# Optimization experiments

Measured on AMD Instinct MI355X. Metric: run time of the kernel, lower is better.

The kernel has to match this reference:

```python
import jax, jax.numpy as jnp
import numpy as np

B, T, C, H, W = 2, 2048, 2048, 16, 512
D = C // H  # head_dim = 128

def setup_inputs() -> dict:
    key = jax.random.key(0)
    k1, k2, k3 = jax.random.split(key, 3)
    x = jax.random.normal(k1, (B, T, C), dtype=jnp.float32)
    w_attn = jax.random.normal(k2, (C, 3 * C), dtype=jnp.float32) * 0.02
    w_proj = jax.random.normal(k3, (C, C), dtype=jnp.float32) * 0.02
    # standard RoPE tables: [T, D] with halves repeated
    inv_freq = 1.0 / (10000.0 ** (jnp.arange(0, D, 2, dtype=jnp.float32) / D))
    freqs = jnp.outer(jnp.arange(T, dtype=jnp.float32), inv_freq)  # [T, D/2]
    emb = jnp.concatenate([freqs, freqs], axis=-1)  # [T, D]
    return {"x": x, "freqs_cos": jnp.cos(emb), "freqs_sin": jnp.sin(emb),
            "w_attn": w_attn, "w_proj": w_proj}

def _rotate_half(t):
    return jnp.concatenate([-t[..., D // 2:], t[..., :D // 2]], axis=-1)

def reference(x, freqs_cos, freqs_sin, w_attn, w_proj):
    qkv = x @ w_attn  # [B,T,3C]
    q, k, v = jnp.split(qkv, 3, axis=-1)
    # [B,T,C] -> [B,H,T,D]
    q = q.reshape(B, T, H, D).transpose(0, 2, 1, 3)
    k = k.reshape(B, T, H, D).transpose(0, 2, 1, 3)
    v = v.reshape(B, T, H, D).transpose(0, 2, 1, 3)
    cos = freqs_cos[None, None, :, :]  # [1,1,T,D]
    sin = freqs_sin[None, None, :, :]
    q = q * cos + _rotate_half(q) * sin
    k = k * cos + _rotate_half(k) * sin
    scores = jnp.einsum('bhqd,bhkd->bhqk', q, k) / jnp.sqrt(jnp.float32(D))
    i = jnp.arange(T)[:, None]
    j = jnp.arange(T)[None, :]
    band = (j <= i) & (j > i - W)  # causal sliding window of width W
    scores = jnp.where(band[None, None, :, :], scores, -jnp.inf)
    att = jax.nn.softmax(scores, axis=-1)
    y = jnp.einsum('bhqk,bhkd->bhqd', att, v)
    y = y.transpose(0, 2, 1, 3).reshape(B, T, C)
    return y @ w_proj
```

## Files before the change

kernel.cpp:

```cpp
#include <hip/hip_runtime.h>
#include <stdint.h>

#define B_ 2
#define T_ 2048
#define C_ 2048
#define H_ 16
#define D_ 128
#define W_ 512
#define M_ (B_*T_)
#define N1_ (3*C_)

typedef short bf16x8 __attribute__((ext_vector_type(8)));
typedef unsigned short u16x8 __attribute__((ext_vector_type(8)));
typedef float f32x4 __attribute__((ext_vector_type(4)));

#define SB() __builtin_amdgcn_sched_barrier(0)

__device__ __forceinline__ unsigned short f2bf(float f) {
  union { float f; unsigned u; } v; v.f = f;
  unsigned r = v.u + 0x7fffu + ((v.u >> 16) & 1u);
  return (unsigned short)(r >> 16);
}
__device__ __forceinline__ float bf2f(unsigned short b) {
  union { unsigned u; float f; } v; v.u = ((unsigned)b) << 16;
  return v.f;
}

__device__ __forceinline__ void gload_lds16(const void* g, void* l) {
  __builtin_amdgcn_global_load_lds((const __attribute__((address_space(1))) void*)g,
                                   (__attribute__((address_space(3))) void*)l, 16, 0, 0);
}

__global__ void k_cvt(const float* __restrict__ s, unsigned short* __restrict__ d, int n) {
  int i = (blockIdx.x * blockDim.x + threadIdx.x) * 8;
  if (i >= n) return;
  float4 a = *(const float4*)(s + i);
  float4 b = *(const float4*)(s + i + 4);
  u16x8 o;
  o[0]=f2bf(a.x); o[1]=f2bf(a.y); o[2]=f2bf(a.z); o[3]=f2bf(a.w);
  o[4]=f2bf(b.x); o[5]=f2bf(b.y); o[6]=f2bf(b.z); o[7]=f2bf(b.w);
  *(u16x8*)(d + i) = o;
}

__global__ void k_tcvt(const float* __restrict__ s, unsigned short* __restrict__ d, int R, int Cc) {
  __shared__ float tile[32][33];
  int c0 = blockIdx.x * 32, r0 = blockIdx.y * 32;
  int tx = threadIdx.x & 31, ty = threadIdx.x >> 5;
  #pragma unroll
  for (int j = 0; j < 32; j += 8) tile[ty + j][tx] = s[(size_t)(r0 + ty + j) * Cc + c0 + tx];
  __syncthreads();
  #pragma unroll
  for (int j = 0; j < 32; j += 8) d[(size_t)(c0 + ty + j) * R + r0 + tx] = f2bf(tile[tx][ty + j]);
}

template<int ROWS, int K>
__device__ __forceinline__ void stage_half(const unsigned short* __restrict__ gbase,
                                           int row0, int kt, int kh,
                                           unsigned short* region, int tid, int sw) {
  const char* gsrc = (const char*)(gbase + (size_t)row0 * K + kt * 64 + kh * 32);
  {
    int o = tid * 16, s = o ^ sw;
    gload_lds16(gsrc + (size_t)(s >> 6) * (K * 2) + (s & 63), (char*)region + o);
  }
  if (ROWS == 256) {
    int o = (512 + tid) * 16, s = o ^ sw;
    gload_lds16(gsrc + (size_t)(s >> 6) * (K * 2) + (s & 63), (char*)region + o);
  }
}

template<bool F32OUT, int K, int Ntot>
__global__ __launch_bounds__(512, 2) void k_gemm8(const unsigned short* __restrict__ A,
                                                  const unsigned short* __restrict__ Bt,
                                                  void* __restrict__ Cp) {
  __shared__ unsigned short As[2][2][256 * 32];
  __shared__ unsigned short Bs[2][2][256 * 32];
  const int tid = threadIdx.x, lane = tid & 63, wv = tid >> 6;
  const int wm = wv >> 2, wn = wv & 3;
  const int lr = lane & 15, lg = lane >> 4;
  const int sw = tid & 32;
  const int fofs = lr * 64 + ((lg * 16) ^ ((lr & 8) << 2));
  const int aoff = wm * 128 * 64 + fofs;
  const int boff = wn * 64 * 64 + fofs;

  const int nwg = gridDim.x;
  const int nbx = Ntot >> 8;
  const int q = nwg >> 3, r = nwg & 7;
  const int xcd = blockIdx.x & 7, off = blockIdx.x >> 3;
  const int bid = (xcd < r ? xcd * (q + 1) : r * (q + 1) + (xcd - r) * q) + off;
  const int bm0 = (bid / nbx) << 8;
  const int bn0 = (bid % nbx) << 8;

  f32x4 acc[8][4];
  #pragma unroll
  for (int i = 0; i < 8; ++i)
    #pragma unroll
    for (int j = 0; j < 4; ++j)
      #pragma unroll
      for (int e = 0; e < 4; ++e) acc[i][j][e] = 0.f;

  constexpr int NT = K >> 6;

  stage_half<256, K>(A,  bm0, 0, 0, As[0][0], tid, sw);
  stage_half<256, K>(Bt, bn0, 0, 0, Bs[0][0], tid, sw);
  stage_half<256, K>(Bt, bn0, 0, 1, Bs[0][1], tid, sw);
  stage_half<256, K>(A,  bm0, 0, 1, As[0][1], tid, sw);
  stage_half<256, K>(Bt, bn0, 1, 0, Bs[1][0], tid, sw);
  stage_half<256, K>(A,  bm0, 1, 0, As[1][0], tid, sw);
  stage_half<256, K>(Bt, bn0, 1, 1, Bs[1][1], tid, sw);
  asm volatile("s_waitcnt vmcnt(4)" ::: "memory");
  __builtin_amdgcn_s_barrier();

  bf16x8 Xa[4], Xb[4], Ya[4];
  #pragma unroll
  for (int j = 0; j < 4; ++j) Xb[j] = *(const bf16x8*)((const char*)Bs[0][0] + boff + j * 1024);
  #pragma unroll
  for (int i = 0; i < 4; ++i) Xa[i] = *(const bf16x8*)((const char*)As[0][0] + aoff + i * 1024);

  #pragma unroll 2
  for (int t = 0; t < NT; ++t) {
    const int p = t & 1;
    asm volatile("s_waitcnt lgkmcnt(0)" ::: "memory");
    SB();
    __builtin_amdgcn_s_setprio(1);
    #pragma unroll
    for (int i = 0; i < 4; ++i)
      #pragma unroll
      for (int j = 0; j < 4; ++j)
        acc[i][j] = __builtin_amdgcn_mfma_f32_16x16x32_bf16(Xa[i], Xb[j], acc[i][j], 0, 0, 0);
    __builtin_amdgcn_s_setprio(0);
    #pragma unroll
    for (int i = 0; i < 4; ++i) Ya[i] = *(const bf16x8*)((const char*)As[p][0] + aoff + (i + 4) * 1024);
    if (t + 1 < NT) stage_half<256, K>(A, bm0, t + 1, 1, As[p ^ 1][1], tid, sw);
    __builtin_amdgcn_s_barrier();

    asm volatile("s_waitcnt lgkmcnt(0)" ::: "memory");
    SB();
    __builtin_amdgcn_s_setprio(1);
    #pragma unroll
    for (int i = 0; i < 4; ++i)
      #pragma unroll
      for (int j = 0; j < 4; ++j)
        acc[i + 4][j] = __builtin_amdgcn_mfma_f32_16x16x32_bf16(Ya[i], Xb[j], acc[i + 4][j], 0, 0, 0);
    __builtin_amdgcn_s_setprio(0);
    #pragma unroll
    for (int j = 0; j < 4; ++j) Xb[j] = *(const bf16x8*)((const char*)Bs[p][1] + boff + j * 1024);
    #pragma unroll
    for (int i = 0; i < 4; ++i) Xa[i] = *(const bf16x8*)((const char*)As[p][1] + aoff + i * 1024);
    if (t + 2 < NT) stage_half<256, K>(Bt, bn0, t + 2, 0, Bs[p][0], tid, sw);
    __builtin_amdgcn_s_barrier();

    asm volatile("s_waitcnt lgkmcnt(0)" ::: "memory");
    SB();
    __builtin_amdgcn_s_setprio(1);
    #pragma unroll
    for (int i = 0; i < 4; ++i)
      #pragma unroll
      for (int j = 0; j < 4; ++j)
        acc[i][j] = __builtin_amdgcn_mfma_f32_16x16x32_bf16(Xa[i], Xb[j], acc[i][j], 0, 0, 0);
    __builtin_amdgcn_s_setprio(0);
    #pragma unroll
    for (int i = 0; i < 4; ++i) Ya[i] = *(const bf16x8*)((const char*)As[p][1] + aoff + (i + 4) * 1024);
    if (t + 2 < NT) stage_half<256, K>(A, bm0, t + 2, 0, As[p][0], tid, sw);
    __builtin_amdgcn_s_barrier();

    asm volatile("s_waitcnt lgkmcnt(0)" ::: "memory");
    SB();
    __builtin_amdgcn_s_setprio(1);
    #pragma unroll
    for (int i = 0; i < 4; ++i)
      #pragma unroll
      for (int j = 0; j < 4; ++j)
        acc[i + 4][j] = __builtin_amdgcn_mfma_f32_16x16x32_bf16(Ya[i], Xb[j], acc[i + 4][j], 0, 0, 0);
    __builtin_amdgcn_s_setprio(0);
    if (t < NT - 2) asm volatile("s_waitcnt vmcnt(4)" ::: "memory");
    else            asm volatile("s_waitcnt vmcnt(0)" ::: "memory");
    #pragma unroll
    for (int j = 0; j < 4; ++j) Xb[j] = *(const bf16x8*)((const char*)Bs[p ^ 1][0] + boff + j * 1024);
    #pragma unroll
    for (int i = 0; i < 4; ++i) Xa[i] = *(const bf16x8*)((const char*)As[p ^ 1][0] + aoff + i * 1024);
    if (t + 2 < NT) stage_half<256, K>(Bt, bn0, t + 2, 1, Bs[p][1], tid, sw);
    __builtin_amdgcn_s_barrier();
  }
  asm volatile("s_waitcnt lgkmcnt(0)" ::: "memory");

  #pragma unroll
  for (int i = 0; i < 8; ++i)
    #pragma unroll
    for (int j = 0; j < 4; ++j) {
      int m = bm0 + wm * 128 + i * 16 + lg * 4;
      int n = bn0 + wn * 64 + j * 16 + lr;
      #pragma unroll
      for (int e = 0; e < 4; ++e) {
        if (F32OUT) ((float*)Cp)[(size_t)(m + e) * Ntot + n] = acc[i][j][e];
        else ((unsigned short*)Cp)[(size_t)(m + e) * Ntot + n] = f2bf(acc[i][j][e]);
      }
    }
}

template<bool F32OUT, int K, int Ntot>
__global__ __launch_bounds__(512, 1) void k_gemmT(const unsigned short* __restrict__ A,
                                                  const unsigned short* __restrict__ Bt,
                                                  void* __restrict__ Cp) {
  __shared__ unsigned short As[3][2][128 * 32];
  __shared__ unsigned short Bs[3][2][256 * 32];
  const int tid = threadIdx.x, lane = tid & 63, wv = tid >> 6;
  const int wm = wv >> 2, wn = wv & 3;
  const int lr = lane & 15, lg = lane >> 4;
  const int sw = tid & 32;
  const int fofs = lr * 64 + ((lg * 16) ^ ((lr & 8) << 2));
  const int aoff = wm * 64 * 64 + fofs;
  const int boff = wn * 64 * 64 + fofs;

  const int nwg = gridDim.x;
  const int nbx = Ntot >> 8;
  const int q = nwg >> 3, r = nwg & 7;
  const int xcd = blockIdx.x & 7, off = blockIdx.x >> 3;
  const int bid = (xcd < r ? xcd * (q + 1) : r * (q + 1) + (xcd - r) * q) + off;
  const int bm0 = (bid / nbx) * 128;
  const int bn0 = (bid % nbx) << 8;

  f32x4 acc[4][4];
  #pragma unroll
  for (int i = 0; i < 4; ++i)
    #pragma unroll
    for (int j = 0; j < 4; ++j)
      #pragma unroll
      for (int e = 0; e < 4; ++e) acc[i][j][e] = 0.f;

  constexpr int NT = K >> 6;

  auto stage_tile = [&](int kt, int rr) {
    stage_half<128, K>(A,  bm0, kt, 0, As[rr][0], tid, sw);
    stage_half<256, K>(Bt, bn0, kt, 0, Bs[rr][0], tid, sw);
    stage_half<128, K>(A,  bm0, kt, 1, As[rr][1], tid, sw);
    stage_half<256, K>(Bt, bn0, kt, 1, Bs[rr][1], tid, sw);
  };

  stage_tile(0, 0);
  stage_tile(1, 1);
  asm volatile("s_waitcnt vmcnt(6)" ::: "memory");
  __builtin_amdgcn_s_barrier();
  bf16x8 Pf[4], Qf[4], Xf[4], Yf[4];
  #pragma unroll
  for (int i = 0; i < 4; ++i) Pf[i] = *(const bf16x8*)((const char*)As[0][0] + aoff + i * 1024);
  #pragma unroll
  for (int j = 0; j < 4; ++j) Xf[j] = *(const bf16x8*)((const char*)Bs[0][0] + boff + j * 1024);

  int cur = 0;
  for (int t = 0; t < NT; ++t) {
    int rn = cur + 1; if (rn == 3) rn = 0;
    int rs = rn + 1; if (rs == 3) rs = 0;

    asm volatile("s_waitcnt lgkmcnt(0)" ::: "memory");
    SB();
    __builtin_amdgcn_s_setprio(1);
    #pragma unroll
    for (int i = 0; i < 4; ++i)
      #pragma unroll
      for (int j = 0; j < 4; ++j)
        acc[i][j] = __builtin_amdgcn_mfma_f32_16x16x32_bf16(Pf[i], Xf[j], acc[i][j], 0, 0, 0);
    __builtin_amdgcn_s_setprio(0);
    #pragma unroll
    for (int i = 0; i < 4; ++i) Qf[i] = *(const bf16x8*)((const char*)As[cur][1] + aoff + i * 1024);
    #pragma unroll
    for (int j = 0; j < 4; ++j) Yf[j] = *(const bf16x8*)((const char*)Bs[cur][1] + boff + j * 1024);
    if (t + 2 < NT) {
      stage_tile(t + 2, rs);
      asm volatile("s_waitcnt vmcnt(9)" ::: "memory");
    } else if (t + 1 < NT) {
      asm volatile("s_waitcnt vmcnt(3)" ::: "memory");
    } else {
      asm volatile("s_waitcnt vmcnt(0)" ::: "memory");
    }
    __builtin_amdgcn_s_barrier();

    asm volatile("s_waitcnt lgkmcnt(0)" ::: "memory");
    SB();
    __builtin_amdgcn_s_setprio(1);
    #pragma unroll
    for (int i = 0; i < 4; ++i)
      #pragma unroll
      for (int j = 0; j < 4; ++j)
        acc[i][j] = __builtin_amdgcn_mfma_f32_16x16x32_bf16(Qf[i], Yf[j], acc[i][j], 0, 0, 0);
    __builtin_amdgcn_s_setprio(0);
    if (t + 1 < NT) {
      #pragma unroll
      for (int i = 0; i < 4; ++i) Pf[i] = *(const bf16x8*)((const char*)As[rn][0] + aoff + i * 1024);
      #pragma unroll
      for (int j = 0; j < 4; ++j) Xf[j] = *(const bf16x8*)((const char*)Bs[rn][0] + boff + j * 1024);
    }
    if (t + 2 < NT) asm volatile("s_waitcnt vmcnt(6)" ::: "memory");
    else            asm volatile("s_waitcnt vmcnt(0)" ::: "memory");
    __builtin_amdgcn_s_barrier();

    cur = rn;
  }
  asm volatile("s_waitcnt lgkmcnt(0)" ::: "memory");

  #pragma unroll
  for (int i = 0; i < 4; ++i)
    #pragma unroll
    for (int j = 0; j < 4; ++j) {
      int m = bm0 + wm * 64 + i * 16 + lg * 4;
      int n = bn0 + wn * 64 + j * 16 + lr;
      #pragma unroll
      for (int e = 0; e < 4; ++e) {
        if (F32OUT) ((float*)Cp)[(size_t)(m + e) * Ntot + n] = acc[i][j][e];
        else ((unsigned short*)Cp)[(size_t)(m + e) * Ntot + n] = f2bf(acc[i][j][e]);
      }
    }
}

__global__ __launch_bounds__(256) void k_reorg(const unsigned short* __restrict__ qkv,
                        const float* __restrict__ fcos, const float* __restrict__ fsin,
                        unsigned short* __restrict__ q_r, unsigned short* __restrict__ k_r,
                        unsigned short* __restrict__ v_t) {
  const int bh = blockIdx.x, b = bh >> 4, h = bh & 15;
  const int t0 = blockIdx.y * 64;
  const int tid = threadIdx.x;
  __shared__ unsigned short vt[64][136];
  #pragma unroll
  for (int p = 0; p < 4; ++p) {
    int idx = p * 256 + tid;
    int tl = idx >> 4, sg = idx & 15;
    int t = t0 + tl, d0 = sg * 8;
    float sgn = (d0 < 64) ? -1.f : 1.f;
    float4 c0v = *(const float4*)(fcos + t * D_ + d0);
    float4 c1v = *(const float4*)(fcos + t * D_ + d0 + 4);
    float4 s0v = *(const float4*)(fsin + t * D_ + d0);
    float4 s1v = *(const float4*)(fsin + t * D_ + d0 + 4);
    float cs[8] = {c0v.x,c0v.y,c0v.z,c0v.w,c1v.x,c1v.y,c1v.z,c1v.w};
    float sn[8] = {s0v.x,s0v.y,s0v.z,s0v.w,s1v.x,s1v.y,s1v.z,s1v.w};
    #pragma unroll
    for (int w = 0; w < 2; ++w) {
      const unsigned short* src = qkv + (size_t)(b*T_ + t) * N1_ + w*C_ + h*D_;
      u16x8 a  = *(const u16x8*)(src + d0);
      u16x8 pr = *(const u16x8*)(src + (d0 ^ 64));
      u16x8 o;
      #pragma unroll
      for (int e = 0; e < 8; ++e)
        o[e] = f2bf(bf2f(a[e]) * cs[e] + sgn * bf2f(pr[e]) * sn[e]);
      unsigned short* dst = (w ? k_r : q_r) + (size_t)((b*H_ + h)*T_ + t) * D_ + d0;
      *(u16x8*)dst = o;
    }
    const unsigned short* vsrc = qkv + (size_t)(b*T_ + t) * N1_ + 2*C_ + h*D_ + d0;
    *(u16x8*)&vt[tl][d0] = *(const u16x8*)vsrc;
  }
  __syncthreads();
  #pragma unroll
  for (int p = 0; p < 4; ++p) {
    int idx = p * 256 + tid;
    int sg = idx & 7, d = idx >> 3;
    u16x8 o;
    #pragma unroll
    for (int e = 0; e < 8; ++e) o[e] = vt[sg*8 + e][d];
    *(u16x8*)(v_t + (size_t)((b*H_ + h)*D_ + d) * T_ + t0 + sg*8) = o;
  }
}

__global__ __launch_bounds__(512) void k_attn(const unsigned short* __restrict__ q_r,
                       const unsigned short* __restrict__ k_r,
                       const unsigned short* __restrict__ v_t,
                       unsigned short* __restrict__ y) {
  const int bh = blockIdx.x, b = bh >> 4, h = bh & 15;
  const int q0 = blockIdx.y * 128;
  const int tid = threadIdx.x, lane = tid & 63, wv = tid >> 6;
  const int lr = lane & 15, lg = lane >> 4;

  __shared__ unsigned short Ks[2][64 * 128];
  __shared__ unsigned short Vs[128 * 64];
  __shared__ unsigned short Ps[8 * 16 * 64];

  const size_t bhT = (size_t)(b*H_ + h) * T_;
  const size_t bhD = (size_t)(b*H_ + h) * D_;
  const unsigned short* qbase = q_r + (bhT + q0 + wv*16 + lr) * D_;
  bf16x8 qf[4];
  #pragma unroll
  for (int kk = 0; kk < 4; ++kk) qf[kk] = *(const bf16x8*)(qbase + kk*32 + lg*8);

  f32x4 o[8];
  #pragma unroll
  for (int i = 0; i < 8; ++i)
    #pragma unroll
    for (int e = 0; e < 4; ++e) o[i][e] = 0.f;
  float m_run[4], l_sum[4];
  #pragma unroll
  for (int e = 0; e < 4; ++e) { m_run[e] = -1e30f; l_sum[e] = 0.f; }

  const int i_min = q0 + wv*16, i_max = i_min + 15;
  int kt_lo = q0 - (W_ - 1); if (kt_lo < 0) kt_lo = 0; kt_lo &= ~63;
  const float scale = 0.08838834764831845f;

  unsigned short* Ps_w = Ps + wv * 1024;

  auto stage_k = [&](int kt, int buf) {
    #pragma unroll
    for (int c = 0; c < 2; ++c) {
      int ob = (c * 512 + tid) * 16;
      int row = ob >> 8, slot = (ob >> 4) & 15;
      int cb = slot ^ ((row & 7) << 1);
      gload_lds16(k_r + (bhT + kt + row) * D_ + cb * 8, (char*)Ks[buf] + ob);
    }
  };
  auto stage_v = [&](int kt) {
    #pragma unroll
    for (int c = 0; c < 2; ++c) {
      int ob = (c * 512 + tid) * 16;
      int d = ob >> 7, slot = (ob >> 4) & 7;
      int cb = slot ^ (d & 7);
      gload_lds16(v_t + (bhD + d) * T_ + kt + cb * 8, (char*)Vs + ob);
    }
  };

  stage_k(kt_lo, 0);
  int cur = 0;
  for (int kt = kt_lo; kt < q0 + 128; kt += 64) {
    const bool has_next = (kt + 64 < q0 + 128);
    stage_v(kt);
    if (has_next) stage_k(kt + 64, cur ^ 1);
    if (has_next) asm volatile("s_waitcnt vmcnt(4)" ::: "memory");
    else          asm volatile("s_waitcnt vmcnt(2)" ::: "memory");
    __builtin_amdgcn_s_barrier();

    const bool live = (kt <= i_max) && (kt + 63 >= i_min - (W_ - 1));
    float sv[4][4];
    if (live) {
      const unsigned short* Kc = Ks[cur];
      f32x4 s[4];
      #pragma unroll
      for (int ct = 0; ct < 4; ++ct)
        #pragma unroll
        for (int e = 0; e < 4; ++e) s[ct][e] = 0.f;
      #pragma unroll
      for (int kk = 0; kk < 4; ++kk) {
        #pragma unroll
        for (int ct = 0; ct < 4; ++ct) {
          bf16x8 kf = *(const bf16x8*)&Kc[(ct*16 + lr)*128 + ((kk*4 + lg) ^ ((lr & 7) << 1))*8];
          s[ct] = __builtin_amdgcn_mfma_f32_16x16x32_bf16(qf[kk], kf, s[ct], 0, 0, 0);
        }
      }
      float mnew[4];
      int grow = 0;
      #pragma unroll
      for (int e = 0; e < 4; ++e) {
        int i = i_min + lg*4 + e;
        float rm = -1e30f;
        #pragma unroll
        for (int ct = 0; ct < 4; ++ct) {
          int j = kt + ct*16 + lr;
          bool ok = (j <= i) && (j > i - W_);
          sv[e][ct] = ok ? s[ct][e] * scale : -1e30f;
          rm = fmaxf(rm, sv[e][ct]);
        }
        #pragma unroll
        for (int msk = 1; msk < 16; msk <<= 1) rm = fmaxf(rm, __shfl_xor(rm, msk));
        mnew[e] = fmaxf(m_run[e], rm);
        grow |= (mnew[e] > m_run[e]) ? 1 : 0;
      }
      if (__any(grow)) {
        #pragma unroll
        for (int e = 0; e < 4; ++e) {
          float fac = __expf(m_run[e] - mnew[e]);
          l_sum[e] *= fac;
          m_run[e] = mnew[e];
          #pragma unroll
          for (int nt = 0; nt < 8; ++nt) o[nt][e] *= fac;
        }
      }
      #pragma unroll
      for (int e = 0; e < 4; ++e) {
        int prow = lg*4 + e;
        float rs = 0.f;
        #pragma unroll
        for (int ct = 0; ct < 4; ++ct) {
          float pv = (sv[e][ct] > -1e29f) ? __expf(sv[e][ct] - m_run[e]) : 0.f;
          rs += pv;
          Ps_w[prow*64 + ((ct*2 + (lr >> 3)) ^ (prow & 7))*8 + (lr & 7)] = f2bf(pv);
        }
        #pragma unroll
        for (int msk = 1; msk < 16; msk <<= 1) rs += __shfl_xor(rs, msk);
        l_sum[e] += rs;
      }
    }
    if (has_next) asm volatile("s_waitcnt vmcnt(2)" ::: "memory");
    else          asm volatile("s_waitcnt vmcnt(0)" ::: "memory");
    __builtin_amdgcn_s_barrier();

    if (live) {
      asm volatile("s_waitcnt lgkmcnt(0)" ::: "memory"); SB();
      #pragma unroll
      for (int kk = 0; kk < 2; ++kk) {
        bf16x8 pf = *(const bf16x8*)&Ps_w[lr*64 + ((kk*4 + lg) ^ (lr & 7))*8];
        #pragma unroll
        for (int nt = 0; nt < 8; ++nt) {
          bf16x8 vf = *(const bf16x8*)&Vs[(nt*16 + lr)*64 + ((kk*4 + lg) ^ (lr & 7))*8];
          o[nt] = __builtin_amdgcn_mfma_f32_16x16x32_bf16(pf, vf, o[nt], 0, 0, 0);
        }
      }
    }
    asm volatile("s_waitcnt lgkmcnt(0)" ::: "memory");
    __builtin_amdgcn_s_barrier();
    cur ^= 1;
  }

  #pragma unroll
  for (int nt = 0; nt < 8; ++nt) {
    #pragma unroll
    for (int e = 0; e < 4; ++e) {
      int t = q0 + wv*16 + lg*4 + e;
      int d = nt*16 + lr;
      y[(size_t)(b*T_ + t) * C_ + h*D_ + d] = f2bf(o[nt][e] / l_sum[e]);
    }
  }
}

extern "C" void kernel_launch(void* const* d_in, const int* in_sizes, int n_in,
                              void* d_out, int out_size, void* d_ws, size_t ws_size,
                              hipStream_t stream) {
  const float* x      = (const float*)d_in[0];
  const float* fcos   = (const float*)d_in[1];
  const float* fsin   = (const float*)d_in[2];
  const float* w_attn = (const float*)d_in[3];
  const float* w_proj = (const float*)d_in[4];
  float* out = (float*)d_out;

  char* ws = (char*)d_ws;
  unsigned short* x_bf = (unsigned short*)(ws);
  unsigned short* wa_t = (unsigned short*)(ws + 16777216ull);
  unsigned short* wp_t = (unsigned short*)(ws + 41943040ull);
  unsigned short* qkv  = (unsigned short*)(ws + 50331648ull);
  unsigned short* q_r  = (unsigned short*)(ws + 100663296ull);
  unsigned short* k_r  = (unsigned short*)(ws + 117440512ull);
  unsigned short* v_t  = (unsigned short*)(ws + 134217728ull);
  unsigned short* y_bf = x_bf;

  k_cvt<<<dim3(4096), dim3(256), 0, stream>>>(x, x_bf, M_*C_);
  k_tcvt<<<dim3(192, 64), dim3(256), 0, stream>>>(w_attn, wa_t, C_, N1_);
  k_tcvt<<<dim3(64, 64), dim3(256), 0, stream>>>(w_proj, wp_t, C_, C_);
  k_gemm8<false, C_, N1_><<<dim3(384), dim3(512), 0, stream>>>(x_bf, wa_t, qkv);
  k_reorg<<<dim3(32, 32), dim3(256), 0, stream>>>(qkv, fcos, fsin, q_r, k_r, v_t);
  k_attn<<<dim3(32, 16), dim3(512), 0, stream>>>(q_r, k_r, v_t, y_bf);
  k_gemmT<true, C_, C_><<<dim3(256), dim3(512), 0, stream>>>(y_bf, wp_t, out);
}
```

Baseline: 283.3 us.

## Replace output projection GEMM with smaller 128x128 tile double-buffered kernel

The output projection GEMM moves from a 128x256 tile with a 3-stage software-pipelined register-prefetch loop to a 128x128 tile with a simple 2-stage LDS double buffer. The grid doubles to 512 workgroups and launch bounds allow several blocks per CU. The aim is to spread the 4096x2048 GEMM across more workgroups (256 only roughly matches the CU count) and gain occupancy-based latency hiding. The cost is losing the explicit register prefetch and vmcnt-overlapped scheduling, plus lower per-tile data reuse.

```diff
diff --git a/kernel.cpp b/kernel.cpp
--- a/kernel.cpp
+++ b/kernel.cpp
@@ -197,31 +197,31 @@
     }
 }
 
-template<bool F32OUT, int K, int Ntot>
-__global__ __launch_bounds__(512, 1) void k_gemmT(const unsigned short* __restrict__ A,
+template<int K, int Ntot>
+__global__ __launch_bounds__(512, 4) void k_gemmS(const unsigned short* __restrict__ A,
                                                   const unsigned short* __restrict__ Bt,
-                                                  void* __restrict__ Cp) {
-  __shared__ unsigned short As[3][2][128 * 32];
-  __shared__ unsigned short Bs[3][2][256 * 32];
+                                                  float* __restrict__ Cp) {
+  __shared__ unsigned short As[2][2][128 * 32];
+  __shared__ unsigned short Bs[2][2][128 * 32];
   const int tid = threadIdx.x, lane = tid & 63, wv = tid >> 6;
-  const int wm = wv >> 2, wn = wv & 3;
+  const int wm = wv >> 1, wn = wv & 1;
   const int lr = lane & 15, lg = lane >> 4;
   const int sw = tid & 32;
   const int fofs = lr * 64 + ((lg * 16) ^ ((lr & 8) << 2));
-  const int aoff = wm * 64 * 64 + fofs;
+  const int aoff = wm * 32 * 64 + fofs;
   const int boff = wn * 64 * 64 + fofs;
 
   const int nwg = gridDim.x;
-  const int nbx = Ntot >> 8;
+  const int nbx = Ntot >> 7;
   const int q = nwg >> 3, r = nwg & 7;
   const int xcd = blockIdx.x & 7, off = blockIdx.x >> 3;
   const int bid = (xcd < r ? xcd * (q + 1) : r * (q + 1) + (xcd - r) * q) + off;
-  const int bm0 = (bid / nbx) * 128;
-  const int bn0 = (bid % nbx) << 8;
-
-  f32x4 acc[4][4];
-  #pragma unroll
-  for (int i = 0; i < 4; ++i)
+  const int bm0 = (bid / nbx) << 7;
+  const int bn0 = (bid % nbx) << 7;
+
+  f32x4 acc[2][4];
+  #pragma unroll
+  for (int i = 0; i < 2; ++i)
     #pragma unroll
     for (int j = 0; j < 4; ++j)
       #pragma unroll
@@ -231,83 +231,49 @@
 
   auto stage_tile = [&](int kt, int rr) {
     stage_half<128, K>(A,  bm0, kt, 0, As[rr][0], tid, sw);
-    stage_half<256, K>(Bt, bn0, kt, 0, Bs[rr][0], tid, sw);
+    stage_half<128, K>(Bt, bn0, kt, 0, Bs[rr][0], tid, sw);
     stage_half<128, K>(A,  bm0, kt, 1, As[rr][1], tid, sw);
-    stage_half<256, K>(Bt, bn0, kt, 1, Bs[rr][1], tid, sw);
+    stage_half<128, K>(Bt, bn0, kt, 1, Bs[rr][1], tid, sw);
   };
 
   stage_tile(0, 0);
-  stage_tile(1, 1);
-  asm volatile("s_waitcnt vmcnt(6)" ::: "memory");
+  asm volatile("s_waitcnt vmcnt(0)" ::: "memory");
   __builtin_amdgcn_s_barrier();
-  bf16x8 Pf[4], Qf[4], Xf[4], Yf[4];
-  #pragma unroll
-  for (int i = 0; i < 4; ++i) Pf[i] = *(const bf16x8*)((const char*)As[0][0] + aoff + i * 1024);
-  #pragma unroll
-  for (int j = 0; j < 4; ++j) Xf[j] = *(const bf16x8*)((const char*)Bs[0][0] + boff + j * 1024);
-
-  int cur = 0;
+
   for (int t = 0; t < NT; ++t) {
-    int rn = cur + 1; if (rn == 3) rn = 0;
-    int rs = rn + 1; if (rs == 3) rs = 0;
-
-    asm volatile("s_waitcnt lgkmcnt(0)" ::: "memory");
-    SB();
-    __builtin_amdgcn_s_setprio(1);
-    #pragma unroll
-    for (int i = 0; i < 4; ++i)
-      #pragma unroll
-      for (int j = 0; j < 4; ++j)
-        acc[i][j] = __builtin_amdgcn_mfma_f32_16x16x32_bf16(Pf[i], Xf[j], acc[i][j], 0, 0, 0);
-    __builtin_amdgcn_s_setprio(0);
-    #pragma unroll
-    for (int i = 0; i < 4; ++i) Qf[i] = *(const bf16x8*)((const char*)As[cur][1] + aoff + i * 1024);
-    #pragma unroll
-    for (int j = 0; j < 4; ++j) Yf[j] = *(const bf16x8*)((const char*)Bs[cur][1] + boff + j * 1024);
-    if (t + 2 < NT) {
-      stage_tile(t + 2, rs);
-      asm volatile("s_waitcnt vmcnt(9)" ::: "memory");
-    } else if (t + 1 < NT) {
-      asm volatile("s_waitcnt vmcnt(3)" ::: "memory");
-    } else {
-      asm volatile("s_waitcnt vmcnt(0)" ::: "memory");
-    }
-    __builtin_amdgcn_s_barrier();
-
-    asm volatile("s_waitcnt lgkmcnt(0)" ::: "memory");
-    SB();
-    __builtin_amdgcn_s_setprio(1);
-    #pragma unroll
-    for (int i = 0; i < 4; ++i)
-      #pragma unroll
-      for (int j = 0; j < 4; ++j)
-        acc[i][j] = __builtin_amdgcn_mfma_f32_16x16x32_bf16(Qf[i], Yf[j], acc[i][j], 0, 0, 0);
-    __builtin_amdgcn_s_setprio(0);
-    if (t + 1 < NT) {
-      #pragma unroll
-      for (int i = 0; i < 4; ++i) Pf[i] = *(const bf16x8*)((const char*)As[rn][0] + aoff + i * 1024);
-      #pragma unroll
-      for (int j = 0; j < 4; ++j) Xf[j] = *(const bf16x8*)((const char*)Bs[rn][0] + boff + j * 1024);
-    }
-    if (t + 2 < NT) asm volatile("s_waitcnt vmcnt(6)" ::: "memory");
-    else            asm volatile("s_waitcnt vmcnt(0)" ::: "memory");
-    __builtin_amdgcn_s_barrier();
-
-    cur = rn;
-  }
-  asm volatile("s_waitcnt lgkmcnt(0)" ::: "memory");
-
-  #pragma unroll
-  for (int i = 0; i < 4; ++i)
+    const int p = t & 1;
+    if (t + 1 < NT) stage_tile(t + 1, p ^ 1);
+
+    bf16x8 af[2], bfr[4];
+    #pragma unroll
+    for (int kh = 0; kh < 2; ++kh) {
+      #pragma unroll
+      for (int i = 0; i < 2; ++i) af[i] = *(const bf16x8*)((const char*)As[p][kh] + aoff + i * 1024);
+      #pragma unroll
+      for (int j = 0; j < 4; ++j) bfr[j] = *(const bf16x8*)((const char*)Bs[p][kh] + boff + j * 1024);
+      asm volatile("s_waitcnt lgkmcnt(0)" ::: "memory");
+      SB();
+      __builtin_amdgcn_s_setprio(1);
+      #pragma unroll
+      for (int i = 0; i < 2; ++i)
+        #pragma unroll
+        for (int j = 0; j < 4; ++j)
+          acc[i][j] = __builtin_amdgcn_mfma_f32_16x16x32_bf16(af[i], bfr[j], acc[i][j], 0, 0, 0);
+      __builtin_amdgcn_s_setprio(0);
+    }
+    asm volatile("s_waitcnt vmcnt(0)" ::: "memory");
+    __builtin_amdgcn_s_barrier();
+  }
+
+  #pragma unroll
+  for (int i = 0; i < 2; ++i)
     #pragma unroll
     for (int j = 0; j < 4; ++j) {
-      int m = bm0 + wm * 64 + i * 16 + lg * 4;
+      int m = bm0 + wm * 32 + i * 16 + lg * 4;
       int n = bn0 + wn * 64 + j * 16 + lr;
       #pragma unroll
-      for (int e = 0; e < 4; ++e) {
-        if (F32OUT) ((float*)Cp)[(size_t)(m + e) * Ntot + n] = acc[i][j][e];
-        else ((unsigned short*)Cp)[(size_t)(m + e) * Ntot + n] = f2bf(acc[i][j][e]);
-      }
+      for (int e = 0; e < 4; ++e)
+        Cp[(size_t)(m + e) * Ntot + n] = acc[i][j][e];
     }
 }
 
@@ -540,5 +506,5 @@
   k_gemm8<false, C_, N1_><<<dim3(384), dim3(512), 0, stream>>>(x_bf, wa_t, qkv);
   k_reorg<<<dim3(32, 32), dim3(256), 0, stream>>>(qkv, fcos, fsin, q_r, k_r, v_t);
   k_attn<<<dim3(32, 16), dim3(512), 0, stream>>>(q_r, k_r, v_t, y_bf);
-  k_gemmT<true, C_, C_><<<dim3(256), dim3(512), 0, stream>>>(y_bf, wp_t, out);
-}
+  k_gemmS<C_, C_><<<dim3(512), dim3(512), 0, stream>>>(y_bf, wp_t, out);
+}
```

Result: no change. 282.1 us (-0.4%).
